# Kernel optimization log

Measured on AMD Instinct MI355X. Metric: run time of the kernel, lower is better.

The kernel has to match this reference:

```python
import jax, jax.numpy as jnp
import numpy as np
from jax import lax

SCALE = 4
KSIZE = 5
NUM_RES = 12


def conv2d(x, w, b):
    # x: [B,C,H,W], w: [O,I,3,3], stride 1, SAME padding
    y = lax.conv_general_dilated(x, w, (1, 1), 'SAME',
                                 dimension_numbers=('NCHW', 'OIHW', 'NCHW'))
    return y + b[None, :, None, None]


def pixel_shuffle(x, r):
    B, C, H, W = x.shape
    c = C // (r * r)
    x = x.reshape(B, c, r, r, H, W)
    x = x.transpose(0, 1, 4, 2, 5, 3)  # B,c,H,r,W,r
    return x.reshape(B, c, H * r, W * r)


def local_conv_us(img, kernel, scale, k):
    B, C, H, W = img.shape
    # im2col patches, channel-major feature ordering (C, k, k) like F.unfold
    patches = lax.conv_general_dilated_patches(img, (k, k), (1, 1), 'SAME')
    patches = patches.reshape(B, C, k * k, H, W)
    kern = kernel.reshape(B, k * k, scale * scale, H, W)
    # kernel_normalize: zero-mean over k*k axis, then add 1/(k*k)
    kern = kern - jnp.mean(kern, axis=1, keepdims=True) + 1.0 / (k * k)
    # per-pixel dynamic filtering: sum over k*k taps
    out = jnp.einsum('bckhw,bkshw->bcshw', patches, kern)
    # manual pixel shuffle of the s*s axis
    out = out.reshape(B, C, scale, scale, H, W)
    out = out.transpose(0, 1, 4, 2, 5, 3)  # B,C,H,s,W,s
    return out.reshape(B, C, H * scale, W * scale)


def setup_inputs() -> dict:
    key = jax.random.key(0)
    ks = jax.random.split(key, 12)
    s = 0.05
    inp = {
        'x': jax.random.normal(ks[0], (4, 3, 128, 128), jnp.float32),
        'w_in': jax.random.normal(ks[1], (64, 3, 3, 3), jnp.float32) * s,
        'b_in': jnp.zeros((64,), jnp.float32),
        'res_w1': jax.random.normal(ks[2], (NUM_RES, 64, 64, 3, 3), jnp.float32) * s,
        'res_b1': jnp.zeros((NUM_RES, 64), jnp.float32),
        'res_w2': jax.random.normal(ks[3], (NUM_RES, 64, 64, 3, 3), jnp.float32) * s,
        'res_b2': jnp.zeros((NUM_RES, 64), jnp.float32),
        'r_w1': jax.random.normal(ks[4], (128, 64, 3, 3), jnp.float32) * s,
        'r_b1': jnp.zeros((128,), jnp.float32),
        'r_w2': jax.random.normal(ks[5], (64, 32, 3, 3), jnp.float32) * s,
        'r_b2': jnp.zeros((64,), jnp.float32),
        'r_w3': jax.random.normal(ks[6], (3, 16, 3, 3), jnp.float32) * s,
        'r_b3': jnp.zeros((3,), jnp.float32),
        'k_w1': jax.random.normal(ks[7], (128, 64, 3, 3), jnp.float32) * s,
        'k_b1': jnp.zeros((128,), jnp.float32),
        'k_w2': jax.random.normal(ks[8], (400, 128, 3, 3), jnp.float32) * s,
        'k_b2': jnp.zeros((400,), jnp.float32),
    }
    return inp


def reference(x, w_in, b_in, res_w1, res_b1, res_w2, res_b2,
              r_w1, r_b1, r_w2, r_b2, r_w3, r_b3,
              k_w1, k_b1, k_w2, k_b2):
    # shared body
    f = conv2d(x, w_in, b_in)
    for i in range(NUM_RES):
        h = conv2d(jax.nn.relu(f), res_w1[i], res_b1[i])
        h = conv2d(jax.nn.relu(h), res_w2[i], res_b2[i])
        f = f + h
    f = jax.nn.relu(f)
    # residual branch: conv->relu->PS2->conv->relu->PS2->conv
    r = pixel_shuffle(jax.nn.relu(conv2d(f, r_w1, r_b1)), 2)
    r = pixel_shuffle(jax.nn.relu(conv2d(r, r_w2, r_b2)), 2)
    residual_img = conv2d(r, r_w3, r_b3)
    # kernel branch
    k = jax.nn.relu(conv2d(f, k_w1, k_b1))
    up_kernel = conv2d(k, k_w2, k_b2)  # [B, 400, H, W]
    upsampled = local_conv_us(x, up_kernel, SCALE, KSIZE)
    return upsampled + residual_img
```

## Files before the change

### kernel.cpp

```cpp
#include <hip/hip_runtime.h>
#include <stdint.h>

typedef __attribute__((ext_vector_type(8))) __bf16 bf16x8;
typedef __attribute__((ext_vector_type(4))) float f32x4;

__device__ __forceinline__ f32x4 MFMA(bf16x8 a, bf16x8 b, f32x4 c) {
    return __builtin_amdgcn_mfma_f32_16x16x32_bf16(a, b, c, 0, 0, 0);
}

struct WSeg { const float* src; int off, OC, IC; };
struct WTab { WSeg s[28]; };

__global__ __launch_bounds__(256) void wcvt_k(WTab tab, __bf16* dst, int seg0) {
    const WSeg sg = tab.s[seg0 + blockIdx.y];
    int n = sg.OC * sg.IC * 9;
    int e = blockIdx.x * 256 + threadIdx.x;
    if (e >= n) return;
    int ic9 = sg.IC * 9;
    int oc = e / ic9;
    int r  = e - oc * ic9;
    int ic = r / 9;
    int t  = r - ic * 9;
    dst[(size_t)sg.off + ((size_t)t * sg.OC + oc) * sg.IC + ic] = (__bf16)sg.src[e];
}

__global__ __launch_bounds__(256) void conv_in_k(
    const float* __restrict__ x, const float* __restrict__ w,
    const float* __restrict__ bias, __bf16* __restrict__ out)
{
    const int tid = threadIdx.x;
    const int ty = (blockIdx.x >> 3) * 16, tx = (blockIdx.x & 7) * 16;
    const int b = blockIdx.y;
    __shared__ float xs[3][18][18];
    __shared__ float wl[27][64];
    for (int i = tid; i < 27 * 64; i += 256) {
        int t = i >> 6, oc = i & 63;
        wl[t][oc] = w[oc * 27 + t];
    }
    for (int i = tid; i < 3 * 324; i += 256) {
        int c = i / 324, r = i - c * 324;
        int y = r / 18, xx = r - y * 18;
        int gy = ty + y - 1, gx = tx + xx - 1;
        float v = 0.f;
        if (gy >= 0 && gy < 128 && gx >= 0 && gx < 128)
            v = x[((size_t)(b * 3 + c) * 128 + gy) * 128 + gx];
        xs[c][y][xx] = v;
    }
    __syncthreads();
    const int py = tid >> 4, px = tid & 15;
    float acc[64];
#pragma unroll
    for (int o = 0; o < 64; o++) acc[o] = bias[o];
    for (int c = 0; c < 3; c++)
        for (int t = 0; t < 9; t++) {
            float p = xs[c][py + t / 3][px + t % 3];
            const float* wr = &wl[c * 9 + t][0];
#pragma unroll
            for (int o = 0; o < 64; o++) acc[o] = fmaf(p, wr[o], acc[o]);
        }
    __bf16* op = out + (((size_t)b * 16384) + (ty + py) * 128 + (tx + px)) * 64;
    for (int o = 0; o < 64; o += 8) {
        union { bf16x8 v; uint4 u; } pk;
#pragma unroll
        for (int j = 0; j < 8; j++) pk.v[j] = (__bf16)acc[o + j];
        *(uint4*)(op + o) = pk.u;
    }
}

template<int CIN, int ICB, int MT, int STAGE, int OUTM,
         bool RELU_IN, bool RELU_OUT, bool ACCUM, bool OCGUARD>
__global__ __launch_bounds__(256) void convm_k(
    const __bf16* __restrict__ in, const __bf16* __restrict__ wt,
    const float* __restrict__ bias, void* __restrict__ outv,
    int H, int W, int OCALL, int ocb0)
{
    constexpr int M = MT * 16;
    constexpr int CHUNKS = CIN / ICB;
    constexpr int GR = ICB / 8;
    constexpr int GM = (GR >= 8 ? 7 : GR - 1);
    constexpr int KS = ICB / 32;

    const int tid = threadIdx.x;
    const int ntx = W >> 4;
    const int q = gridDim.x >> 3;
    const int tile = (blockIdx.x & 7) * q + (blockIdx.x >> 3);
    const int h0 = (tile / ntx) << 4;
    const int w0 = (tile % ntx) << 4;
    const int b = blockIdx.y;
    const int ocb = ocb0 + blockIdx.z * M;

    __shared__ __bf16 inT[324 * ICB];
    __shared__ __bf16 wT[9 * M * ICB];

    const int lane = tid & 63;
    const int wv = tid >> 6;
    const int cl = lane & 15;
    const int kg = lane >> 4;
    const int row0 = wv << 2;

#define SWZ(g, r) (((g) & ~GM) | (((g) ^ (r) ^ ((r) >> 2)) & GM))

    f32x4 acc[MT][4];
#pragma unroll
    for (int m = 0; m < MT; m++) {
        f32x4 bv;
#pragma unroll
        for (int j = 0; j < 4; j++) {
            int o = ocb + m * 16 + kg * 4 + j;
            bv[j] = (!OCGUARD || o < OCALL) ? bias[o] : 0.f;
        }
#pragma unroll
        for (int n = 0; n < 4; n++) acc[m][n] = bv;
    }

    for (int c = 0; c < CHUNKS; c++) {
        if (c) __syncthreads();
        if (STAGE == 0) {
            for (int i = tid; i < 324 * GR; i += 256) {
                int pix = i / GR, g = i - pix * GR;
                int y = pix / 18, xx = pix - y * 18;
                int gy = h0 + y - 1, gx = w0 + xx - 1;
                union { uint4 u; bf16x8 v; unsigned short us[8]; } d;
                d.u = make_uint4(0u, 0u, 0u, 0u);
                if (gy >= 0 && gy < H && gx >= 0 && gx < W) {
                    d.u = *(const uint4*)(in + (((size_t)(b * H + gy)) * W + gx) * CIN
                                          + c * ICB + g * 8);
                    if (RELU_IN) {
#pragma unroll
                        for (int j = 0; j < 8; j++)
                            if (d.us[j] & 0x8000u) d.us[j] = 0;
                    }
                }
                int sg = SWZ(g, pix);
                *(bf16x8*)(inT + pix * ICB + sg * 8) = d.v;
            }
        } else {
            const int SRCH = H >> 1, SRCW = W >> 1, SRCC = 4 * CIN;
            constexpr int NG = ICB / 2;
            for (int i = tid; i < 324 * NG; i += 256) {
                int pix = i / NG, g = i - pix * NG;
                int y = pix / 18, xx = pix - y * 18;
                int gy = h0 + y - 1, gx = w0 + xx - 1;
                union { uint4 u; __bf16 hx[8]; } d;
                d.u = make_uint4(0u, 0u, 0u, 0u);
                int sub = 0;
                if (gy >= 0 && gy < H && gx >= 0 && gx < W) {
                    sub = ((gy & 1) << 1) | (gx & 1);
                    d.u = *(const uint4*)(in
                        + (((size_t)(b * SRCH + (gy >> 1))) * SRCW + (gx >> 1)) * SRCC
                        + c * ICB * 4 + g * 8);
                }
                __bf16 v0 = d.hx[sub], v1 = d.hx[4 + sub];
                int e0 = 2 * g;
                int gr = e0 >> 3;
                int sg = SWZ(gr, pix);
                inT[pix * ICB + sg * 8 + (e0 & 7)] = v0;
                inT[pix * ICB + sg * 8 + ((e0 & 7) + 1)] = v1;
            }
        }
        for (int i = tid; i < 9 * M * GR; i += 256) {
            int t = i / (M * GR), r = i - t * (M * GR);
            int oc = r / GR, g = r - oc * GR;
            int ocr = ocb + oc;
            if (OCGUARD) ocr = (ocr < OCALL) ? ocr : (OCALL - 1);
            union { uint4 u; bf16x8 v; } d;
            d.u = *(const uint4*)(wt + ((size_t)t * OCALL + ocr) * CIN
                                  + c * ICB + g * 8);
            int sg = SWZ(g, oc);
            *(bf16x8*)(wT + ((t * M) + oc) * ICB + sg * 8) = d.v;
        }
        __syncthreads();

#pragma unroll
        for (int t = 0; t < 9; t++) {
            const int dy = t / 3, dx = t % 3;
            const __bf16* wb = wT + t * M * ICB;
#pragma unroll
            for (int ks = 0; ks < KS; ks++) {
                bf16x8 af[MT], bfr[4];
#pragma unroll
                for (int m = 0; m < MT; m++) {
                    int oc = m * 16 + cl;
                    int g = ks * 4 + kg;
                    int sg = SWZ(g, oc);
                    af[m] = *(const bf16x8*)(wb + oc * ICB + sg * 8);
                }
#pragma unroll
                for (int n = 0; n < 4; n++) {
                    int pix = (row0 + n + dy) * 18 + cl + dx;
                    int g = ks * 4 + kg;
                    int sg = SWZ(g, pix);
                    bfr[n] = *(const bf16x8*)(inT + pix * ICB + sg * 8);
                }
#pragma unroll
                for (int m = 0; m < MT; m++)
#pragma unroll
                    for (int n = 0; n < 4; n++)
                        acc[m][n] = MFMA(af[m], bfr[n], acc[m][n]);
            }
        }
    }
#undef SWZ

    if (OUTM == 0) {
        __bf16* outp = (__bf16*)outv;
#pragma unroll
        for (int m = 0; m < MT; m++) {
            int oc = ocb + m * 16 + kg * 4;
            if (!OCGUARD || oc < OCALL) {
#pragma unroll
                for (int n = 0; n < 4; n++) {
                    __bf16* op = outp + (((size_t)(b * H + h0 + row0 + n)) * W + (w0 + cl))
                                     * OCALL + oc;
                    f32x4 v = acc[m][n];
                    if (ACCUM) {
                        union { uint2 u; __bf16 hx[4]; } old;
                        old.u = *(const uint2*)op;
#pragma unroll
                        for (int j = 0; j < 4; j++) v[j] += (float)old.hx[j];
                    }
                    union { uint2 u; __bf16 hx[4]; } pk;
#pragma unroll
                    for (int j = 0; j < 4; j++) {
                        float f = v[j];
                        if (RELU_OUT) f = fmaxf(f, 0.f);
                        pk.hx[j] = (__bf16)f;
                    }
                    *(uint2*)op = pk.u;
                }
            }
        }
    } else {
        __bf16* outp = (__bf16*)outv;
        const int HW = H * W;
        const int CP = OCALL >> 2;
#pragma unroll
        for (int m = 0; m < MT; m++) {
            int cc = (ocb + m * 16 + kg * 4) >> 2;
#pragma unroll
            for (int n = 0; n < 4; n++) {
                int pix = (h0 + row0 + n) * W + w0 + cl;
#pragma unroll
                for (int j = 0; j < 4; j++) {
                    float f = acc[m][n][j];
                    if (RELU_OUT) f = fmaxf(f, 0.f);
                    outp[((size_t)(b * 4 + j) * HW + pix) * CP + cc] = (__bf16)f;
                }
            }
        }
    }
}

__global__ __launch_bounds__(256) void rw3_k(
    const __bf16* __restrict__ r2p, const float* __restrict__ w,
    const float* __restrict__ bias, float* __restrict__ E)
{
    const int tid = threadIdx.x;
    const int tY = (blockIdx.x >> 4) * 16;
    const int tX = (blockIdx.x & 15) * 16;
    const int b = blockIdx.y;

    __shared__ __bf16 xs[4][18][18][16];
    __shared__ float wl[3][9][16];
    for (int i = tid; i < 432; i += 256) {
        int oc = i / 144, r = i - oc * 144;
        int t = r >> 4, e = r & 15;
        wl[oc][t][e] = w[(oc * 16 + e) * 9 + t];
    }
    for (int i = tid; i < 4 * 18 * 36; i += 256) {
        int g = i % 36; int r = i / 36;
        int y = r % 18, sub = r / 18;
        int px = g >> 1, half = g & 1;
        int gy = tY + y - 1, gx = tX + px - 1;
        uint4 v = make_uint4(0u, 0u, 0u, 0u);
        if (gy >= 0 && gy < 256 && gx >= 0 && gx < 256)
            v = *(const uint4*)(r2p
                + (((size_t)(b * 4 + sub) << 16) + (gy << 8) + gx) * 16 + half * 8);
        *(uint4*)(&xs[sub][y][px][half * 8]) = v;
    }
    __syncthreads();

    const int hyl = tid >> 3;
    const int hx0 = (tid & 7) * 4;
    float acc[3][4];
#pragma unroll
    for (int oc = 0; oc < 3; oc++)
#pragma unroll
        for (int p = 0; p < 4; p++) acc[oc][p] = bias[oc];

#pragma unroll
    for (int dy = 0; dy < 3; dy++) {
        int hy = hyl + dy - 1;
        int ys = (hy >> 1) + 1;
        int suby = (hy & 1) << 1;
#pragma unroll
        for (int dx = 0; dx < 3; dx++) {
            const int t = dy * 3 + dx;
#pragma unroll
            for (int p = 0; p < 4; p++) {
                int hx = hx0 + p + dx - 1;
                int sub = suby | (hx & 1);
                int xsx = (hx >> 1) + 1;
                const __bf16* bp = &xs[sub][ys][xsx][0];
                bf16x8 v0 = *(const bf16x8*)bp;
                bf16x8 v1 = *(const bf16x8*)(bp + 8);
#pragma unroll
                for (int e = 0; e < 8; e++) {
                    float f0 = (float)v0[e], f1 = (float)v1[e];
                    acc[0][p] = fmaf(f0, wl[0][t][e], acc[0][p]);
                    acc[1][p] = fmaf(f0, wl[1][t][e], acc[1][p]);
                    acc[2][p] = fmaf(f0, wl[2][t][e], acc[2][p]);
                    acc[0][p] = fmaf(f1, wl[0][t][e + 8], acc[0][p]);
                    acc[1][p] = fmaf(f1, wl[1][t][e + 8], acc[1][p]);
                    acc[2][p] = fmaf(f1, wl[2][t][e + 8], acc[2][p]);
                }
            }
        }
    }
    const int HY = tY * 2 + hyl, HX = tX * 2 + hx0;
#pragma unroll
    for (int oc = 0; oc < 3; oc++) {
        float4 v = make_float4(acc[oc][0], acc[oc][1], acc[oc][2], acc[oc][3]);
        *(float4*)&E[(((size_t)(b * 3 + oc)) << 18) + HY * 512 + HX] = v;
    }
}

__global__ __launch_bounds__(256) void filter_k(
    const __bf16* __restrict__ Ut, const float* __restrict__ x,
    const float* __restrict__ E, float* __restrict__ out)
{
    const int tid = threadIdx.x;
    const int s  = tid >> 4;
    const int pl = tid & 15;
    const int b  = blockIdx.y;
    const int pix0 = blockIdx.x * 16;
    const int y  = pix0 >> 7;
    const int x0 = pix0 & 127;

    __shared__ float xp[3][5][20];
    __shared__ float vs[3][16][16];
    __shared__ __bf16 ut[16][408];

    for (int i = tid; i < 800; i += 256) {
        int px = i / 50, g = i - px * 50;
        uint4 v = *(const uint4*)(Ut + ((size_t)(b * 16384 + pix0 + px) * 400 + g * 8));
        *(uint4*)(&ut[px][g * 8]) = v;
    }
    for (int i = tid; i < 300; i += 256) {
        int c = i / 100, r = i - c * 100;
        int dy = r / 20, dx = r - dy * 20;
        int gy = y + dy - 2, gx = x0 + dx - 2;
        float v = 0.f;
        if (gy >= 0 && gy < 128 && gx >= 0 && gx < 128)
            v = x[((size_t)(b * 3 + c) * 128 + gy) * 128 + gx];
        xp[c][dy][dx] = v;
    }
    __syncthreads();

    float u[25], m = 0.f;
#pragma unroll
    for (int tap = 0; tap < 25; tap++) {
        u[tap] = (float)ut[pl][tap * 16 + s];
        m += u[tap];
    }
    m *= 0.04f;
#pragma unroll
    for (int c = 0; c < 3; c++) {
        float a = 0.f;
#pragma unroll
        for (int tap = 0; tap < 25; tap++)
            a = fmaf(xp[c][tap / 5][pl + tap % 5], u[tap] - m + 0.04f, a);
        vs[c][s][pl] = a;
    }
    __syncthreads();

    const size_t Eb = (size_t)b * 3 * 262144;
    for (int i = tid; i < 768; i += 256) {
        int c = i >> 8, r = i & 255;
        int s1 = r >> 6, cc = r & 63;
        float v = vs[c][s1 * 4 + (cc & 3)][cc >> 2];
        size_t o = Eb + (size_t)c * 262144 + (size_t)(y * 4 + s1) * 512 + x0 * 4 + cc;
        out[o] = v + E[o];
    }
}

extern "C" void kernel_launch(void* const* d_in, const int* in_sizes, int n_in,
                              void* d_out, int out_size, void* d_ws, size_t ws_size,
                              hipStream_t stream)
{
    const float* x      = (const float*)d_in[0];
    const float* w_in   = (const float*)d_in[1];
    const float* b_in   = (const float*)d_in[2];
    const float* res_w1 = (const float*)d_in[3];
    const float* res_b1 = (const float*)d_in[4];
    const float* res_w2 = (const float*)d_in[5];
    const float* res_b2 = (const float*)d_in[6];
    const float* r_w1   = (const float*)d_in[7];
    const float* r_b1   = (const float*)d_in[8];
    const float* r_w2   = (const float*)d_in[9];
    const float* r_b2   = (const float*)d_in[10];
    const float* r_w3   = (const float*)d_in[11];
    const float* r_b3   = (const float*)d_in[12];
    const float* k_w1   = (const float*)d_in[13];
    const float* k_b1   = (const float*)d_in[14];
    const float* k_w2   = (const float*)d_in[15];
    const float* k_b2   = (const float*)d_in[16];
    float* out = (float*)d_out;

    char* ws = (char*)d_ws;
    __bf16* WT = (__bf16*)ws;
    __bf16* F  = (__bf16*)(ws + 3145728);
    __bf16* Hb = (__bf16*)(ws + 11534336);
    __bf16* R1 = (__bf16*)(ws + 19922944);
    __bf16* R2 = (__bf16*)(ws + 36700160);
    __bf16* K1 = (__bf16*)(ws + 70254592);
    float*  E  = (float*) (ws + 87031808);
    __bf16* Ut = (__bf16*)(ws + 3145728);

    const int oRes1 = 0, oRes2 = 442368, oRw1 = 884736, oKw1 = 958464,
              oRw2 = 1032192, oKw2 = 1050624;

    WTab tab;
    for (int i = 0; i < 12; i++)
        tab.s[i]      = { res_w1 + (size_t)i * 36864, oRes1 + i * 36864, 64, 64 };
    for (int i = 0; i < 12; i++)
        tab.s[12 + i] = { res_w2 + (size_t)i * 36864, oRes2 + i * 36864, 64, 64 };
    tab.s[24] = { r_w1, oRw1, 128, 64 };
    tab.s[25] = { k_w1, oKw1, 128, 64 };
    tab.s[26] = { r_w2, oRw2, 64, 32 };
    tab.s[27] = { k_w2, oKw2, 400, 128 };

    dim3 blk(256);
    wcvt_k<<<dim3(288, 27), blk, 0, stream>>>(tab, WT, 0);
    wcvt_k<<<dim3(1800, 1), blk, 0, stream>>>(tab, WT, 27);

    conv_in_k<<<dim3(64, 4), blk, 0, stream>>>(x, w_in, b_in, F);

    for (int i = 0; i < 12; i++) {
        convm_k<64, 32, 2, 0, 0, true, true, false, false>
            <<<dim3(64, 4, 2), blk, 0, stream>>>(
            F, WT + oRes1 + i * 36864, res_b1 + i * 64, Hb, 128, 128, 64, 0);
        convm_k<64, 32, 2, 0, 0, false, false, true, false>
            <<<dim3(64, 4, 2), blk, 0, stream>>>(
            Hb, WT + oRes2 + i * 36864, res_b2 + i * 64, F, 128, 128, 64, 0);
    }

    convm_k<64, 32, 2, 0, 0, true, true, false, false>
        <<<dim3(64, 4, 4), blk, 0, stream>>>(
        F, WT + oRw1, r_b1, R1, 128, 128, 128, 0);
    convm_k<32, 32, 2, 1, 2, false, true, false, false>
        <<<dim3(256, 4, 2), blk, 0, stream>>>(
        R1, WT + oRw2, r_b2, R2, 256, 256, 64, 0);
    rw3_k<<<dim3(256, 4), blk, 0, stream>>>(R2, r_w3, r_b3, E);

    convm_k<64, 32, 2, 0, 0, true, true, false, false>
        <<<dim3(64, 4, 4), blk, 0, stream>>>(
        F, WT + oKw1, k_b1, K1, 128, 128, 128, 0);

    convm_k<128, 32, 2, 0, 0, false, false, false, true>
        <<<dim3(64, 4, 13), blk, 0, stream>>>(
        K1, WT + oKw2, k_b2, Ut, 128, 128, 400, 0);

    filter_k<<<dim3(1024, 4), blk, 0, stream>>>(Ut, x, E, out);
}
```

Baseline: 571.5 us.

## Pre-swizzle weights into LDS image and load them with global_load_lds

The weight conversion kernel now writes weights in a per-block, per-chunk pre-swizzled layout that matches the LDS tile exactly, padding the output channels to a multiple of 32. The conv kernel then copies each chunk's weight tile straight from global memory into LDS with the async global_load_lds builtin, so the VGPR round trip, index math and swizzle stores are gone. This relies on M=32 and ICB=32 matching the hardcoded layout in wcvt_k, and it grows the weight buffer for k_w2.

```diff
diff --git a/kernel.cpp b/kernel.cpp
--- a/kernel.cpp
+++ b/kernel.cpp
@@ -8,20 +8,35 @@
     return __builtin_amdgcn_mfma_f32_16x16x32_bf16(a, b, c, 0, 0, 0);
 }
 
-struct WSeg { const float* src; int off, OC, IC; };
+typedef __attribute__((address_space(1))) void gas_void;
+typedef __attribute__((address_space(3))) void las_void;
+__device__ __forceinline__ void gload_lds16(const __bf16* g, __bf16* l) {
+    __builtin_amdgcn_global_load_lds((gas_void*)g, (las_void*)l, 16, 0, 0);
+}
+
+struct WSeg { const float* src; int off, OC, OCP, IC; };
 struct WTab { WSeg s[28]; };
 
 __global__ __launch_bounds__(256) void wcvt_k(WTab tab, __bf16* dst, int seg0) {
     const WSeg sg = tab.s[seg0 + blockIdx.y];
-    int n = sg.OC * sg.IC * 9;
-    int e = blockIdx.x * 256 + threadIdx.x;
-    if (e >= n) return;
-    int ic9 = sg.IC * 9;
-    int oc = e / ic9;
-    int r  = e - oc * ic9;
-    int ic = r / 9;
-    int t  = r - ic * 9;
-    dst[(size_t)sg.off + ((size_t)t * sg.OC + oc) * sg.IC + ic] = (__bf16)sg.src[e];
+    const int n = sg.OCP * sg.IC * 9;
+    int d = blockIdx.x * 256 + threadIdx.x;
+    if (d >= n) return;
+    int q   = d & 31;
+    int r1  = d >> 5;
+    int oc  = r1 & 31;
+    int r2  = r1 >> 5;
+    int t   = r2 % 9;
+    int r3  = r2 / 9;
+    const int CH = sg.IC >> 5;
+    int c   = r3 % CH;
+    int z   = r3 / CH;
+    int sq  = q >> 3, e = q & 7;
+    int g   = (sq ^ oc ^ (oc >> 2)) & 3;
+    int ic  = c * 32 + g * 8 + e;
+    int ocg = z * 32 + oc;
+    float v = (ocg < sg.OC) ? sg.src[((size_t)ocg * sg.IC + ic) * 9 + t] : 0.f;
+    dst[(size_t)sg.off + d] = (__bf16)v;
 }
 
 __global__ __launch_bounds__(256) void conv_in_k(
@@ -79,6 +94,8 @@
     constexpr int GR = ICB / 8;
     constexpr int GM = (GR >= 8 ? 7 : GR - 1);
     constexpr int KS = ICB / 32;
+    constexpr int WELEM = 9 * M * ICB;
+    constexpr int WGRP = WELEM / 512;
 
     const int tid = threadIdx.x;
     const int ntx = W >> 4;
@@ -90,7 +107,7 @@
     const int ocb = ocb0 + blockIdx.z * M;
 
     __shared__ __bf16 inT[324 * ICB];
-    __shared__ __bf16 wT[9 * M * ICB];
+    __shared__ __bf16 wT[WELEM];
 
     const int lane = tid & 63;
     const int wv = tid >> 6;
@@ -98,6 +115,8 @@
     const int kg = lane >> 4;
     const int row0 = wv << 2;
 
+    const __bf16* wimg = wt + (size_t)blockIdx.z * CHUNKS * WELEM;
+
 #define SWZ(g, r) (((g) & ~GM) | (((g) ^ (r) ^ ((r) >> 2)) & GM))
 
     f32x4 acc[MT][4];
@@ -115,6 +134,12 @@
 
     for (int c = 0; c < CHUNKS; c++) {
         if (c) __syncthreads();
+        {
+            const __bf16* wsrc = wimg + (size_t)c * WELEM;
+            for (int j = wv; j < WGRP; j += 4)
+                gload_lds16(wsrc + (size_t)j * 512 + lane * 8,
+                            wT + (size_t)j * 512);
+        }
         if (STAGE == 0) {
             for (int i = tid; i < 324 * GR; i += 256) {
                 int pix = i / GR, g = i - pix * GR;
@@ -157,17 +182,6 @@
                 inT[pix * ICB + sg * 8 + (e0 & 7)] = v0;
                 inT[pix * ICB + sg * 8 + ((e0 & 7) + 1)] = v1;
             }
-        }
-        for (int i = tid; i < 9 * M * GR; i += 256) {
-            int t = i / (M * GR), r = i - t * (M * GR);
-            int oc = r / GR, g = r - oc * GR;
-            int ocr = ocb + oc;
-            if (OCGUARD) ocr = (ocr < OCALL) ? ocr : (OCALL - 1);
-            union { uint4 u; bf16x8 v; } d;
-            d.u = *(const uint4*)(wt + ((size_t)t * OCALL + ocr) * CIN
-                                  + c * ICB + g * 8);
-            int sg = SWZ(g, oc);
-            *(bf16x8*)(wT + ((t * M) + oc) * ICB + sg * 8) = d.v;
         }
         __syncthreads();
 
@@ -422,17 +436,17 @@
 
     WTab tab;
     for (int i = 0; i < 12; i++)
-        tab.s[i]      = { res_w1 + (size_t)i * 36864, oRes1 + i * 36864, 64, 64 };
+        tab.s[i]      = { res_w1 + (size_t)i * 36864, oRes1 + i * 36864, 64, 64, 64 };
     for (int i = 0; i < 12; i++)
-        tab.s[12 + i] = { res_w2 + (size_t)i * 36864, oRes2 + i * 36864, 64, 64 };
-    tab.s[24] = { r_w1, oRw1, 128, 64 };
-    tab.s[25] = { k_w1, oKw1, 128, 64 };
-    tab.s[26] = { r_w2, oRw2, 64, 32 };
-    tab.s[27] = { k_w2, oKw2, 400, 128 };
+        tab.s[12 + i] = { res_w2 + (size_t)i * 36864, oRes2 + i * 36864, 64, 64, 64 };
+    tab.s[24] = { r_w1, oRw1, 128, 128, 64 };
+    tab.s[25] = { k_w1, oKw1, 128, 128, 64 };
+    tab.s[26] = { r_w2, oRw2, 64, 64, 32 };
+    tab.s[27] = { k_w2, oKw2, 400, 416, 128 };
 
     dim3 blk(256);
     wcvt_k<<<dim3(288, 27), blk, 0, stream>>>(tab, WT, 0);
-    wcvt_k<<<dim3(1800, 1), blk, 0, stream>>>(tab, WT, 27);
+    wcvt_k<<<dim3(1872, 1), blk, 0, stream>>>(tab, WT, 27);
 
     conv_in_k<<<dim3(64, 4), blk, 0, stream>>>(x, w_in, b_in, F);
 
```

Result: faster. 529.3 us (-7.4%).
